# Optimization experiments

Hardware: AMD Instinct MI355X
Metric: run time of the kernel (lower is better)

The kernel has to match this reference:

```python
import jax, jax.numpy as jnp
import numpy as np

B = 128        # batch
N = 4096       # FLAGS.network_node
D_IN = 32      # embedding_in_size
D_OUT = 32     # embedding_out_size


def setup_inputs() -> dict:
    key = jax.random.key(0)
    k1, k2, k3, k4 = jax.random.split(key, 4)
    inputs = jax.random.normal(k1, (B, N * D_IN), dtype=jnp.float32)
    # mean-aggregation neighbor matrix: random nonneg, row-normalized (get_neibhour_nodes_matrix_mean)
    raw = jax.random.uniform(k2, (N, N), dtype=jnp.float32)
    adj = raw / jnp.sum(raw, axis=1, keepdims=True)
    # glorot uniform init as in source
    r = np.sqrt(6.0 / (D_IN + D_OUT)).astype(np.float32)
    W_neigh = jax.random.uniform(k3, (D_IN, D_OUT), minval=-r, maxval=r, dtype=jnp.float32)
    W_self = jax.random.uniform(k4, (D_IN, D_OUT), minval=-r, maxval=r, dtype=jnp.float32)
    return {"inputs": inputs, "adj": adj, "W_neigh": W_neigh, "W_self": W_self, "batch_train": 0}


def reference(inputs, adj, W_neigh, W_self, batch_train):
    # Math: relu(x @ (I_N (x) W_self + A (x) W_neigh))
    # Kronecker vec-trick: reshape x to [B, N, D_IN]; then
    #   x @ (A (x) W) reshaped = einsum('bip,ij,pq->bjq', x3, A, W)
    x3 = inputs.reshape(B, N, D_IN)
    self_part = jnp.einsum('bnp,pq->bnq', x3, W_self)            # I_N (x) W_self
    tmp = jnp.einsum('bip,pq->biq', x3, W_neigh)                  # apply small weight first
    neigh_part = jnp.einsum('biq,ij->bjq', tmp, adj)              # aggregate over graph
    out = jax.nn.relu(self_part + neigh_part)
    return out.reshape(B, N * D_OUT)
```

## Files before the change

### kernel.cpp

```cpp
#include <hip/hip_runtime.h>
#include <hip/hip_bf16.h>

#define N_NODES 4096
#define BATCH   128
#define DD      32

typedef float  f32x4  __attribute__((ext_vector_type(4)));
typedef __bf16 bf16x8 __attribute__((ext_vector_type(8)));
typedef int    i32x4  __attribute__((ext_vector_type(4)));
typedef int    i32x8  __attribute__((ext_vector_type(8)));

#define PREP_BLOCKS 2048
#define TR_BLOCKS   4096

__device__ __forceinline__ void async_copy16(const void* g, void* l) {
    __builtin_amdgcn_global_load_lds(
        (const __attribute__((address_space(1))) unsigned int*)g,
        (__attribute__((address_space(3))) unsigned int*)l,
        16, 0, 0);
}

__device__ __forceinline__ unsigned pack_fp8x4(float a, float b, float c, float d) {
    int v = __builtin_amdgcn_cvt_pk_fp8_f32(a, b, 0, false);
    v     = __builtin_amdgcn_cvt_pk_fp8_f32(c, d, v, true);
    return (unsigned)v;
}

__global__ __launch_bounds__(256) void k_pre(
    const float* __restrict__ x, const float* __restrict__ adj,
    const float* __restrict__ Wn, const float* __restrict__ Ws,
    unsigned char* __restrict__ T8, unsigned char* __restrict__ adjT8,
    float* __restrict__ out)
{
    __shared__ float ts[64][65];
    const int tid = threadIdx.x;

    if (blockIdx.x < PREP_BLOCKS) {
        const int lane = tid & 63;
        const int gw   = (blockIdx.x * 256 + tid) >> 6;
        const int m    = lane & 15;
        const int quad = lane >> 4;

        bf16x8 bn[2], bs[2];
#pragma unroll
        for (int h = 0; h < 2; ++h) {
            const int n = m + h * 16;
#pragma unroll
            for (int j = 0; j < 8; ++j) {
                const int k = quad * 8 + j;
                bn[h][j] = (__bf16)Wn[k * 32 + n];
                bs[h][j] = (__bf16)Ws[k * 32 + n];
            }
        }

        for (int t = gw; t < 32768; t += 8192) {
            const int row0 = t << 4;
            const int b    = row0 >> 12;
            const int i0   = row0 & 4095;

            const float4* xp = (const float4*)(x + (size_t)(row0 + m) * DD + quad * 8);
            const float4 x0 = xp[0], x1 = xp[1];
            bf16x8 a;
            a[0] = (__bf16)x0.x; a[1] = (__bf16)x0.y; a[2] = (__bf16)x0.z; a[3] = (__bf16)x0.w;
            a[4] = (__bf16)x1.x; a[5] = (__bf16)x1.y; a[6] = (__bf16)x1.z; a[7] = (__bf16)x1.w;

            const f32x4 z = {};
            const f32x4 cT0 = __builtin_amdgcn_mfma_f32_16x16x32_bf16(a, bn[0], z, 0, 0, 0);
            const f32x4 cT1 = __builtin_amdgcn_mfma_f32_16x16x32_bf16(a, bn[1], z, 0, 0, 0);
            const f32x4 cU0 = __builtin_amdgcn_mfma_f32_16x16x32_bf16(a, bs[0], z, 0, 0, 0);
            const f32x4 cU1 = __builtin_amdgcn_mfma_f32_16x16x32_bf16(a, bs[1], z, 0, 0, 0);

            *(unsigned*)&T8[((size_t)(b * 32 + m))      * N_NODES + i0 + quad * 4] =
                pack_fp8x4(cT0[0], cT0[1], cT0[2], cT0[3]);
            *(unsigned*)&T8[((size_t)(b * 32 + m + 16)) * N_NODES + i0 + quad * 4] =
                pack_fp8x4(cT1[0], cT1[1], cT1[2], cT1[3]);

            float* ub = out + (size_t)b * (N_NODES * DD) + (size_t)(i0 + quad * 4) * DD;
#pragma unroll
            for (int r = 0; r < 4; ++r) {
                ub[r * DD + m]      = cU0[r];
                ub[r * DD + m + 16] = cU1[r];
            }
        }
    } else {
        const int bid = blockIdx.x - PREP_BLOCKS;
        const int cx  = tid & 63;
        const int cy  = tid >> 6;
        const int i0  = (bid >> 6) << 6;
        const int j0  = (bid & 63) << 6;
#pragma unroll
        for (int r = 0; r < 16; ++r) {
            const int row = cy * 16 + r;
            ts[row][cx] = adj[(size_t)(i0 + row) * N_NODES + j0 + cx];
        }
        __syncthreads();
        const int il = (tid & 7) * 8;
        const int jb = tid >> 3;
#pragma unroll
        for (int rr = 0; rr < 2; ++rr) {
            const int jl = jb + rr * 32;
            float v[8];
#pragma unroll
            for (int k = 0; k < 8; ++k) v[k] = ts[il + k][jl] * 4096.0f;
            uint2 p;
            p.x = pack_fp8x4(v[0], v[1], v[2], v[3]);
            p.y = pack_fp8x4(v[4], v[5], v[6], v[7]);
            *(uint2*)&adjT8[(size_t)(j0 + jl) * N_NODES + i0 + il] = p;
        }
    }
}

__global__ __launch_bounds__(256) void k_gemm_neigh(
    const unsigned char* __restrict__ A8,
    const unsigned char* __restrict__ B8,
    float* __restrict__ out)
{
    __shared__ alignas(16) unsigned char As[128 * 128];
    __shared__ alignas(16) unsigned char Bs[128 * 128];

    const int tid   = threadIdx.x;
    const int lane  = tid & 63;
    const int wave  = tid >> 6;
    const int bm    = blockIdx.y << 7;
    const int bn    = blockIdx.x << 7;
    const int waveM = (wave >> 1) << 6;
    const int waveN = (wave & 1) << 6;
    const int lr    = lane & 15;
    const int lq    = lane >> 4;
    const int sw    = lr & 7;

    f32x4 acc[4][4] = {};

    const int srow = tid >> 3;
    const int scol = ((tid & 7) ^ (srow & 7)) * 16;
    const unsigned char* ga = A8 + (size_t)(bm + srow) * 4096 + scol;
    const unsigned char* gb = B8 + (size_t)(bn + srow) * 4096 + scol;
    char* la = (char*)As + tid * 16;
    char* lb = (char*)Bs + tid * 16;

    for (int k0 = 0; k0 < 4096; k0 += 128) {
#pragma unroll
        for (int n = 0; n < 4; ++n) {
            async_copy16(ga + (size_t)(n * 32) * 4096 + k0, la + n * 4096);
            async_copy16(gb + (size_t)(n * 32) * 4096 + k0, lb + n * 4096);
        }
        __syncthreads();

        i32x8 af[4], bfr[4];
#pragma unroll
        for (int t = 0; t < 4; ++t) {
            const int ra = (waveM + t * 16 + lr) * 128;
            const int rb = (waveN + t * 16 + lr) * 128;
            const int c0 = ((2 * lq)     ^ sw) * 16;
            const int c1 = ((2 * lq + 1) ^ sw) * 16;
            const i32x4 alo = *(const i32x4*)&As[ra + c0];
            const i32x4 ahi = *(const i32x4*)&As[ra + c1];
            const i32x4 blo = *(const i32x4*)&Bs[rb + c0];
            const i32x4 bhi = *(const i32x4*)&Bs[rb + c1];
            af[t][0]=alo[0]; af[t][1]=alo[1]; af[t][2]=alo[2]; af[t][3]=alo[3];
            af[t][4]=ahi[0]; af[t][5]=ahi[1]; af[t][6]=ahi[2]; af[t][7]=ahi[3];
            bfr[t][0]=blo[0]; bfr[t][1]=blo[1]; bfr[t][2]=blo[2]; bfr[t][3]=blo[3];
            bfr[t][4]=bhi[0]; bfr[t][5]=bhi[1]; bfr[t][6]=bhi[2]; bfr[t][7]=bhi[3];
        }
#pragma unroll
        for (int tm = 0; tm < 4; ++tm)
#pragma unroll
            for (int tn = 0; tn < 4; ++tn)
                acc[tm][tn] = __builtin_amdgcn_mfma_scale_f32_16x16x128_f8f6f4(
                    af[tm], bfr[tn], acc[tm][tn],
                    0, 0,
                    0, 0x7F,
                    0, 0x73);
        __syncthreads();
    }

#pragma unroll
    for (int tm = 0; tm < 4; ++tm) {
        const int gm0 = bm + waveM + tm * 16 + lq * 4;
        const int b   = gm0 >> 5;
        const int q0  = gm0 & 31;
#pragma unroll
        for (int tn = 0; tn < 4; ++tn) {
            const int gj = bn + waveN + tn * 16 + lr;
            float* p = out + (size_t)b * (N_NODES * DD) + (size_t)gj * DD + q0;
            const float4 u = *(const float4*)p;
            float4 v;
            v.x = fmaxf(acc[tm][tn][0] + u.x, 0.0f);
            v.y = fmaxf(acc[tm][tn][1] + u.y, 0.0f);
            v.z = fmaxf(acc[tm][tn][2] + u.z, 0.0f);
            v.w = fmaxf(acc[tm][tn][3] + u.w, 0.0f);
            *(float4*)p = v;
        }
    }
}

extern "C" void kernel_launch(void* const* d_in, const int* in_sizes, int n_in,
                              void* d_out, int out_size, void* d_ws, size_t ws_size,
                              hipStream_t stream) {
    const float* x   = (const float*)d_in[0];
    const float* adj = (const float*)d_in[1];
    const float* Wn  = (const float*)d_in[2];
    const float* Ws  = (const float*)d_in[3];
    float* out = (float*)d_out;

    unsigned char* T8    = (unsigned char*)d_ws;
    unsigned char* adjT8 = T8 + (size_t)N_NODES * N_NODES;

    hipLaunchKernelGGL(k_pre, dim3(PREP_BLOCKS + TR_BLOCKS), dim3(256), 0, stream,
                       x, adj, Wn, Ws, T8, adjT8, out);
    hipLaunchKernelGGL(k_gemm_neigh, dim3(32, 32), dim3(256), 0, stream, T8, adjT8, out);
}
```

Measured before the change: 273.0 us.

## Double-buffer fp8 GEMM LDS tiles and stage self term in bf16 workspace

```diff
diff --git a/kernel.cpp b/kernel.cpp
--- a/kernel.cpp
+++ b/kernel.cpp
@@ -7,7 +7,8 @@
 
 typedef float  f32x4  __attribute__((ext_vector_type(4)));
 typedef __bf16 bf16x8 __attribute__((ext_vector_type(8)));
-typedef int    i32x4  __attribute__((ext_vector_type(4)));
+typedef __bf16 bf16x4 __attribute__((ext_vector_type(4)));
+typedef int    i32x2  __attribute__((ext_vector_type(2)));
 typedef int    i32x8  __attribute__((ext_vector_type(8)));
 
 #define PREP_BLOCKS 2048
@@ -30,7 +31,7 @@
     const float* __restrict__ x, const float* __restrict__ adj,
     const float* __restrict__ Wn, const float* __restrict__ Ws,
     unsigned char* __restrict__ T8, unsigned char* __restrict__ adjT8,
-    float* __restrict__ out)
+    __bf16* __restrict__ Ub)
 {
     __shared__ float ts[64][65];
     const int tid = threadIdx.x;
@@ -75,23 +76,27 @@
             *(unsigned*)&T8[((size_t)(b * 32 + m + 16)) * N_NODES + i0 + quad * 4] =
                 pack_fp8x4(cT1[0], cT1[1], cT1[2], cT1[3]);
 
-            float* ub = out + (size_t)b * (N_NODES * DD) + (size_t)(i0 + quad * 4) * DD;
+            __bf16* ub = Ub + (size_t)b * (N_NODES * DD) + (size_t)(i0 + quad * 4) * DD;
 #pragma unroll
             for (int r = 0; r < 4; ++r) {
-                ub[r * DD + m]      = cU0[r];
-                ub[r * DD + m + 16] = cU1[r];
+                ub[r * DD + m]      = (__bf16)cU0[r];
+                ub[r * DD + m + 16] = (__bf16)cU1[r];
             }
         }
     } else {
         const int bid = blockIdx.x - PREP_BLOCKS;
-        const int cx  = tid & 63;
-        const int cy  = tid >> 6;
         const int i0  = (bid >> 6) << 6;
         const int j0  = (bid & 63) << 6;
-#pragma unroll
-        for (int r = 0; r < 16; ++r) {
-            const int row = cy * 16 + r;
-            ts[row][cx] = adj[(size_t)(i0 + row) * N_NODES + j0 + cx];
+        const int cr  = tid >> 4;
+        const int cc  = (tid & 15) << 2;
+#pragma unroll
+        for (int it = 0; it < 4; ++it) {
+            const int row = it * 16 + cr;
+            const float4 v = *(const float4*)&adj[(size_t)(i0 + row) * N_NODES + j0 + cc];
+            ts[row][cc]     = v.x;
+            ts[row][cc + 1] = v.y;
+            ts[row][cc + 2] = v.z;
+            ts[row][cc + 3] = v.w;
         }
         __syncthreads();
         const int il = (tid & 7) * 8;
@@ -113,10 +118,11 @@
 __global__ __launch_bounds__(256) void k_gemm_neigh(
     const unsigned char* __restrict__ A8,
     const unsigned char* __restrict__ B8,
+    const __bf16* __restrict__ Ub,
     float* __restrict__ out)
 {
-    __shared__ alignas(16) unsigned char As[128 * 128];
-    __shared__ alignas(16) unsigned char Bs[128 * 128];
+    __shared__ alignas(16) unsigned char As[2][128 * 128];
+    __shared__ alignas(16) unsigned char Bs[2][128 * 128];
 
     const int tid   = threadIdx.x;
     const int lane  = tid & 63;
@@ -129,38 +135,41 @@
     const int lq    = lane >> 4;
     const int sw    = lr & 7;
 
-    f32x4 acc[4][4] = {};
-
     const int srow = tid >> 3;
     const int scol = ((tid & 7) ^ (srow & 7)) * 16;
     const unsigned char* ga = A8 + (size_t)(bm + srow) * 4096 + scol;
     const unsigned char* gb = B8 + (size_t)(bn + srow) * 4096 + scol;
-    char* la = (char*)As + tid * 16;
-    char* lb = (char*)Bs + tid * 16;
-
-    for (int k0 = 0; k0 < 4096; k0 += 128) {
+
+    auto stage = [&](int k0, int buf) {
+        char* la = (char*)&As[buf][0] + tid * 16;
+        char* lb = (char*)&Bs[buf][0] + tid * 16;
 #pragma unroll
         for (int n = 0; n < 4; ++n) {
             async_copy16(ga + (size_t)(n * 32) * 4096 + k0, la + n * 4096);
             async_copy16(gb + (size_t)(n * 32) * 4096 + k0, lb + n * 4096);
         }
-        __syncthreads();
-
+    };
+
+    f32x4 acc[4][4] = {};
+
+    auto compute = [&](int buf) {
         i32x8 af[4], bfr[4];
 #pragma unroll
         for (int t = 0; t < 4; ++t) {
             const int ra = (waveM + t * 16 + lr) * 128;
             const int rb = (waveN + t * 16 + lr) * 128;
-            const int c0 = ((2 * lq)     ^ sw) * 16;
-            const int c1 = ((2 * lq + 1) ^ sw) * 16;
-            const i32x4 alo = *(const i32x4*)&As[ra + c0];
-            const i32x4 ahi = *(const i32x4*)&As[ra + c1];
-            const i32x4 blo = *(const i32x4*)&Bs[rb + c0];
-            const i32x4 bhi = *(const i32x4*)&Bs[rb + c1];
-            af[t][0]=alo[0]; af[t][1]=alo[1]; af[t][2]=alo[2]; af[t][3]=alo[3];
-            af[t][4]=ahi[0]; af[t][5]=ahi[1]; af[t][6]=ahi[2]; af[t][7]=ahi[3];
-            bfr[t][0]=blo[0]; bfr[t][1]=blo[1]; bfr[t][2]=blo[2]; bfr[t][3]=blo[3];
-            bfr[t][4]=bhi[0]; bfr[t][5]=bhi[1]; bfr[t][6]=bhi[2]; bfr[t][7]=bhi[3];
+#pragma unroll
+            for (int j = 0; j < 4; ++j) {
+                const int jp  = (j + lq) & 3;
+                const int g   = 4 * lq + jp;
+                const int off = (((g >> 1) ^ sw) << 4) + ((g & 1) << 3);
+                const i32x2 va = *(const i32x2*)&As[buf][ra + off];
+                const i32x2 vb = *(const i32x2*)&Bs[buf][rb + off];
+                af[t][2 * jp]      = va[0];
+                af[t][2 * jp + 1]  = va[1];
+                bfr[t][2 * jp]     = vb[0];
+                bfr[t][2 * jp + 1] = vb[1];
+            }
         }
 #pragma unroll
         for (int tm = 0; tm < 4; ++tm)
@@ -171,7 +180,16 @@
                     0, 0,
                     0, 0x7F,
                     0, 0x73);
+    };
+
+    stage(0, 0);
+    for (int k0 = 0; k0 < 4096; k0 += 256) {
         __syncthreads();
+        if (k0 + 128 < 4096) stage(k0 + 128, 1);
+        compute(0);
+        __syncthreads();
+        if (k0 + 256 < 4096) stage(k0 + 256, 0);
+        compute(1);
     }
 
 #pragma unroll
@@ -182,14 +200,14 @@
 #pragma unroll
         for (int tn = 0; tn < 4; ++tn) {
             const int gj = bn + waveN + tn * 16 + lr;
-            float* p = out + (size_t)b * (N_NODES * DD) + (size_t)gj * DD + q0;
-            const float4 u = *(const float4*)p;
+            const size_t base = (size_t)b * (N_NODES * DD) + (size_t)gj * DD + q0;
+            const bf16x4 u = *(const bf16x4*)&Ub[base];
             float4 v;
-            v.x = fmaxf(acc[tm][tn][0] + u.x, 0.0f);
-            v.y = fmaxf(acc[tm][tn][1] + u.y, 0.0f);
-            v.z = fmaxf(acc[tm][tn][2] + u.z, 0.0f);
-            v.w = fmaxf(acc[tm][tn][3] + u.w, 0.0f);
-            *(float4*)p = v;
+            v.x = fmaxf(acc[tm][tn][0] + (float)u[0], 0.0f);
+            v.y = fmaxf(acc[tm][tn][1] + (float)u[1], 0.0f);
+            v.z = fmaxf(acc[tm][tn][2] + (float)u[2], 0.0f);
+            v.w = fmaxf(acc[tm][tn][3] + (float)u[3], 0.0f);
+            *(float4*)&out[base] = v;
         }
     }
 }
@@ -205,8 +223,10 @@
 
     unsigned char* T8    = (unsigned char*)d_ws;
     unsigned char* adjT8 = T8 + (size_t)N_NODES * N_NODES;
+    __bf16*        Ubf   = (__bf16*)(adjT8 + (size_t)N_NODES * N_NODES);
 
     hipLaunchKernelGGL(k_pre, dim3(PREP_BLOCKS + TR_BLOCKS), dim3(256), 0, stream,
-                       x, adj, Wn, Ws, T8, adjT8, out);
-    hipLaunchKernelGGL(k_gemm_neigh, dim3(32, 32), dim3(256), 0, stream, T8, adjT8, out);
-}
+                       x, adj, Wn, Ws, T8, adjT8, Ubf);
+    hipLaunchKernelGGL(k_gemm_neigh, dim3(32, 32), dim3(256), 0, stream,
+                       T8, adjT8, Ubf, out);
+}
```

Result: slower. 401.6 us (+47.1%).
